# Optimization experiments

Measured on AMD Instinct MI355X. Metric: run time of the kernel, lower is better.

The kernel has to match this reference:

```python
import jax, jax.numpy as jnp
import numpy as np
from jax import lax

B, CIN, H, W = 32, 256, 64, 64
K, STRIDE = 9, 2
CAPS_TYPES, OS0, OS1 = 32, 8, 1
NUM_ITER = 3
OH = (H - K) // STRIDE + 1  # 28
OW = (W - K) // STRIDE + 1  # 28
EPS = 1e-8


def squash(x):
    # Hinton squash over capsule pose dims (os0, os1)
    n2 = jnp.sum(x * x, axis=(-2, -1), keepdims=True)
    return (n2 / (1.0 + n2)) * x / jnp.sqrt(n2 + EPS)


def setup_inputs() -> dict:
    key = jax.random.key(0)
    k1, k2 = jax.random.split(key)
    x = jax.random.normal(k1, (B, CIN, H, W), jnp.float32)
    cout = CAPS_TYPES * OS0 * OS1
    conv_w = jax.random.normal(k2, (cout, CIN, K, K), jnp.float32) / np.float32(np.sqrt(CIN * K * K))
    conv_b = jnp.zeros((cout,), jnp.float32)
    routing_bias = jnp.full((CAPS_TYPES, OH, OW, OS0, OS1), 0.1, jnp.float32)
    return {"x": x, "conv_w": conv_w, "conv_b": conv_b, "routing_bias": routing_bias}


def reference(x, conv_w, conv_b, routing_bias):
    b = x.shape[0]
    caps = lax.conv_general_dilated(
        x, conv_w, (STRIDE, STRIDE), 'VALID',
        dimension_numbers=('NCHW', 'OIHW', 'NCHW'))
    caps = caps + conv_b[None, :, None, None]
    # [b, C*os0*os1, oh, ow] -> [b, C, oh, ow, os0, os1]
    caps = caps.reshape(b, CAPS_TYPES, OS0, OS1, OH, OW).transpose(0, 1, 4, 5, 2, 3)
    poses = squash(caps)
    # Dynamic routing (degenerate: one vote per output capsule, singleton input dims)
    votes = poses  # [b, C, oh, ow, os0, os1]
    logits = jnp.zeros((b, CAPS_TYPES, OH, OW), caps.dtype)
    for _ in range(NUM_ITER):
        c = jax.nn.softmax(logits, axis=1)           # couplings over output caps types
        s = c[..., None, None] * votes + routing_bias  # weighted vote sum (+ bias)
        poses = squash(s)
        logits = logits + jnp.sum(votes * poses, axis=(-2, -1))  # agreement update
    acts = jnp.sqrt(jnp.sum(poses * poses, axis=(-2, -1)))  # [b, C, oh, ow]
    return poses, acts
```

## Files before the change

kernel.cpp:

```cpp
#include <hip/hip_runtime.h>

#define B_    32
#define CIN_  256
#define H_    64
#define W_    64
#define OH_   28
#define OW_   28
#define M_TOTAL 25088
#define POSE_ELEMS 6422528

typedef _Float16 f16;
typedef _Float16 f16x8 __attribute__((ext_vector_type(8)));
typedef _Float16 f16x4 __attribute__((ext_vector_type(4)));
typedef float    f32x4 __attribute__((ext_vector_type(4)));

#define GLD_LDS16(gp, lp) __builtin_amdgcn_global_load_lds( \
    (const __attribute__((address_space(1))) void*)(gp),    \
    (__attribute__((address_space(3))) void*)(lp), 16, 0, 0)

#define SBAR()    asm volatile("s_barrier" ::: "memory")
#define WAITVM2() asm volatile("s_waitcnt vmcnt(2)" ::: "memory")
#define WAITVM4() asm volatile("s_waitcnt vmcnt(4)" ::: "memory")

__global__ __launch_bounds__(256) void xt_kernel(const float* __restrict__ x,
                                                 f16* __restrict__ Xt)
{
    __shared__ float tile[64 * 65];
    const int t  = threadIdx.x;
    const int c0 = blockIdx.x * 64;
    const int h  = blockIdx.y;
    const int b  = blockIdx.z;

    const float* src = x + (((long)(b * CIN_ + c0)) * H_ + h) * W_;
    const int ci = t >> 6, w = t & 63;
#pragma unroll
    for (int it = 0; it < 16; ++it) {
        const int c = it * 4 + ci;
        tile[c * 65 + w] = src[(long)c * (H_ * W_) + w];
    }
    __syncthreads();

    f16* dst = Xt + ((long)(b * H_ + h) * W_) * CIN_ + c0;
    const int wq = t >> 4, cq = t & 15;
#pragma unroll
    for (int it = 0; it < 4; ++it) {
        const int w2 = it * 16 + wq;
        f16x4 v;
        v[0] = (f16)tile[(cq * 4 + 0) * 65 + w2];
        v[1] = (f16)tile[(cq * 4 + 1) * 65 + w2];
        v[2] = (f16)tile[(cq * 4 + 2) * 65 + w2];
        v[3] = (f16)tile[(cq * 4 + 3) * 65 + w2];
        *(f16x4*)(dst + (long)w2 * CIN_ + cq * 4) = v;
    }
}

__global__ __launch_bounds__(256) void wt_kernel(const float* __restrict__ w,
                                                 f16* __restrict__ Wt)
{
    __shared__ float tile[64 * 81];
    const int t  = threadIdx.x;
    const int co = blockIdx.x >> 2;
    const int c0 = (blockIdx.x & 3) * 64;
    const float* src = w + ((long)co * 256 + c0) * 81;
    for (int i = t; i < 64 * 81; i += 256) tile[i] = src[i];
    __syncthreads();
    for (int i = t; i < 64 * 81; i += 256) {
        const int khw = i >> 6, ci = i & 63;
        Wt[(long)khw * 65536 + co * 256 + c0 + ci] = (f16)tile[ci * 81 + khw];
    }
}

__global__ __launch_bounds__(512, 2) void gemm_kernel(const f16* __restrict__ Xt,
                                                      const f16* __restrict__ Wt,
                                                      float* __restrict__ part,
                                                      int nsplit)
{
    __shared__ __align__(16) char lds[131072];
    char* ldsA = lds;
    char* ldsB = lds + 65536;

    const int t    = threadIdx.x;
    const int lane = t & 63, wave = t >> 6;

    const int nwg = 98 * nsplit;
    const int q = nwg >> 3, r8 = nwg & 7;
    const int xcd = blockIdx.x & 7, idx = blockIdx.x >> 3;
    const int wgid = (xcd < r8 ? xcd * (q + 1) : r8 * (q + 1) + (xcd - r8) * q) + idx;
    const int sk = wgid / 98;
    const int mt = wgid - sk * 98;
    const int m0 = mt * 256;

    const int ntb = 324 / nsplit, rem = 324 - ntb * nsplit;
    const int ksb = sk * ntb + (sk < rem ? sk : rem);
    const int NT  = ntb + (sk < rem ? 1 : 0);

    const int csrc = ((lane & 7) ^ (lane >> 3)) * 8;
    int aoff[4], boff[4];
#pragma unroll
    for (int i = 0; i < 4; ++i) {
        const int r  = (i * 8 + wave) * 8 + (lane >> 3);
        const int ga = (r & 63) + ((r >> 6) & 1) * 128 + (r >> 7) * 64;
        const int m  = m0 + ga;
        const int b   = m / 784;
        const int rem2 = m - b * 784;
        const int oh  = rem2 / 28;
        const int ow  = rem2 - oh * 28;
        aoff[i] = ((b * 64 + 2 * oh) * 64 + 2 * ow) * 256 + csrc;
        const int gb = (r & 31) + ((r >> 5) & 3) * 64 + (r >> 7) * 32;
        boff[i] = gb * 256 + csrc;
    }

    const int wm = wave >> 2, wn = wave & 3;
    int rowA[8], rowB[4];
#pragma unroll
    for (int mf = 0; mf < 8; ++mf) {
        const int g  = wm * 128 + mf * 16 + (lane & 15);
        const int lr = (g & 63) + ((g >> 6) & 1) * 128 + (g >> 7) * 64;
        rowA[mf] = lr * 128;
    }
#pragma unroll
    for (int nf = 0; nf < 4; ++nf) {
        const int g  = wn * 64 + nf * 16 + (lane & 15);
        const int lr = (g & 31) + ((g >> 6) << 5) + ((g >> 5) & 1) * 128;
        rowB[nf] = lr * 128;
    }
    int csw[2];
    csw[0] = ((lane >> 4) * 16) ^ ((lane & 7) << 4);
    csw[1] = 64 ^ csw[0];

    f32x4 acc[8][4];
    const f32x4 z = {0.f, 0.f, 0.f, 0.f};
#pragma unroll
    for (int i = 0; i < 8; ++i)
#pragma unroll
        for (int j = 0; j < 4; ++j) acc[i][j] = z;

#define KOFFS(KS, AK, BK)                                      \
    {  const int cb_ = (KS) & 3, khw_ = (KS) >> 2;             \
       const int kh_ = khw_ / 9, kw_ = khw_ - kh_ * 9;         \
       AK = (kh_ * 64 + kw_) * 256 + cb_ * 64;                 \
       BK = khw_ * 65536 + cb_ * 64; }

#define STAGE_A_HALF(H, AK, NB) do {                                               \
    GLD_LDS16(Xt + aoff[2*(H)]   + (AK), ldsA + (NB)*32768 + ((2*(H))*8   + wave)*1024); \
    GLD_LDS16(Xt + aoff[2*(H)+1] + (AK), ldsA + (NB)*32768 + ((2*(H)+1)*8 + wave)*1024); } while(0)
#define STAGE_B_HALF(H, BK, NB) do {                                               \
    GLD_LDS16(Wt + boff[2*(H)]   + (BK), ldsB + (NB)*32768 + ((2*(H))*8   + wave)*1024); \
    GLD_LDS16(Wt + boff[2*(H)+1] + (BK), ldsB + (NB)*32768 + ((2*(H)+1)*8 + wave)*1024); } while(0)

#define MFMA_PAIR(MI, NI, A, Bf)                                                        \
    acc[MI][NI] = __builtin_amdgcn_mfma_f32_16x16x32_f16((A)[0], (Bf)[0], acc[MI][NI], 0,0,0); \
    acc[MI][NI] = __builtin_amdgcn_mfma_f32_16x16x32_f16((A)[1], (Bf)[1], acc[MI][NI], 0,0,0);
#define MFMA_Q(MH, NH, BF)                                          \
    MFMA_PAIR((MH)*4+0, (NH)*2+0, af[0], BF[0]) MFMA_PAIR((MH)*4+0, (NH)*2+1, af[0], BF[1]) \
    MFMA_PAIR((MH)*4+1, (NH)*2+0, af[1], BF[0]) MFMA_PAIR((MH)*4+1, (NH)*2+1, af[1], BF[1]) \
    MFMA_PAIR((MH)*4+2, (NH)*2+0, af[2], BF[0]) MFMA_PAIR((MH)*4+2, (NH)*2+1, af[2], BF[1]) \
    MFMA_PAIR((MH)*4+3, (NH)*2+0, af[3], BF[0]) MFMA_PAIR((MH)*4+3, (NH)*2+1, af[3], BF[1])

#define READ_AF(P, MH) do {                                           \
    _Pragma("unroll")                                                 \
    for (int k_ = 0; k_ < 4; ++k_) {                                  \
        af[k_][0] = *(const f16x8*)((P) + rowA[(MH)*4+k_] + csw[0]);  \
        af[k_][1] = *(const f16x8*)((P) + rowA[(MH)*4+k_] + csw[1]);  \
    } } while(0)
#define READ_BF(P, V, NH) do {                                        \
    _Pragma("unroll")                                                 \
    for (int k_ = 0; k_ < 2; ++k_) {                                  \
        V[k_][0] = *(const f16x8*)((P) + rowB[(NH)*2+k_] + csw[0]);   \
        V[k_][1] = *(const f16x8*)((P) + rowB[(NH)*2+k_] + csw[1]);   \
    } } while(0)

    f16x8 af[4][2], bf0[2][2], bf1[2][2];

    {
        int ak0, bk0;
        KOFFS(ksb, ak0, bk0);
        STAGE_A_HALF(0, ak0, 0);
        STAGE_B_HALF(0, bk0, 0);
        STAGE_A_HALF(1, ak0, 0);
        STAGE_B_HALF(1, bk0, 0);
    }
    WAITVM4();
    SBAR();
    READ_AF(ldsA, 0);
    READ_BF(ldsB, bf0, 0);

#pragma unroll 1
    for (int tt = 0; tt < NT; ++tt) {
        const int c = tt & 1, nc = c ^ 1;
        const int ksn = ksb + ((tt + 1 < NT) ? tt + 1 : tt);
        int akn, bkn;
        KOFFS(ksn, akn, bkn);
        const char* pA  = ldsA + c * 32768;
        const char* pB  = ldsB + c * 32768;
        const char* pAn = ldsA + nc * 32768;
        const char* pBn = ldsB + nc * 32768;

        STAGE_A_HALF(0, akn, nc);
        WAITVM2();
        SBAR();
        READ_BF(pB, bf1, 1);
        __builtin_amdgcn_s_setprio(1);
        MFMA_Q(0, 0, bf0)
        __builtin_amdgcn_s_setprio(0);

        STAGE_B_HALF(0, bkn, nc);
        SBAR();
        __builtin_amdgcn_s_setprio(1);
        MFMA_Q(0, 1, bf1)
        __builtin_amdgcn_s_setprio(0);
        READ_AF(pA, 1);

        STAGE_A_HALF(1, akn, nc);
        SBAR();
        __builtin_amdgcn_s_setprio(1);
        MFMA_Q(1, 1, bf1)
        __builtin_amdgcn_s_setprio(0);

        STAGE_B_HALF(1, bkn, nc);
        WAITVM4();
        SBAR();
        __builtin_amdgcn_s_setprio(1);
        MFMA_Q(1, 0, bf0)
        __builtin_amdgcn_s_setprio(0);
        READ_AF(pAn, 0);
        READ_BF(pBn, bf0, 0);
    }

    float* base = part + (long)sk * (M_TOTAL * 256);
    const int lrow = (lane >> 4) * 4;
#pragma unroll
    for (int nf = 0; nf < 4; ++nf) {
        const int n = wn * 64 + nf * 16 + (lane & 15);
#pragma unroll
        for (int mf = 0; mf < 8; ++mf) {
            const long mrow = m0 + wm * 128 + mf * 16 + lrow;
            float* cw = base + mrow * 256 + n;
#pragma unroll
            for (int j = 0; j < 4; ++j) cw[(long)j * 256] = acc[mf][nf][j];
        }
    }
}

__global__ __launch_bounds__(256) void routing_kernel(const float* __restrict__ part,
                                                      const float* __restrict__ bias,
                                                      const float* __restrict__ rb,
                                                      float* __restrict__ out, int nsplit)
{
    const int t   = threadIdx.x;
    const int m   = blockIdx.x * 8 + (t >> 5);
    const int cap = t & 31;
    const int b   = m / 784;
    const int rem = m - b * 784;
    const int oh  = rem / 28;
    const int ow  = rem - oh * 28;

    const float4 b0 = ((const float4*)(bias + cap * 8))[0];
    const float4 b1 = ((const float4*)(bias + cap * 8))[1];
    float v[8] = {b0.x, b0.y, b0.z, b0.w, b1.x, b1.y, b1.z, b1.w};
#pragma unroll 1
    for (int sk = 0; sk < nsplit; ++sk) {
        const float4* cp = (const float4*)(part + (long)sk * (M_TOTAL * 256) + (long)m * 256 + cap * 8);
        const float4 u0 = cp[0], u1 = cp[1];
        v[0] += u0.x; v[1] += u0.y; v[2] += u0.z; v[3] += u0.w;
        v[4] += u1.x; v[5] += u1.y; v[6] += u1.z; v[7] += u1.w;
    }

    float n2 = 0.f;
#pragma unroll
    for (int j = 0; j < 8; ++j) n2 += v[j] * v[j];
    const float f = (n2 / (1.f + n2)) / sqrtf(n2 + 1e-8f);
    float votes[8];
#pragma unroll
    for (int j = 0; j < 8; ++j) votes[j] = f * v[j];

    const float4* rp = (const float4*)(rb + ((long)(cap * 28 + oh) * 28 + ow) * 8);
    const float4 r0 = rp[0], r1 = rp[1];
    const float rbv[8] = {r0.x, r0.y, r0.z, r0.w, r1.x, r1.y, r1.z, r1.w};

    float logit = 0.f;
    float poses[8];
#pragma unroll 1
    for (int it = 0; it < 3; ++it) {
        float mx = logit;
#pragma unroll
        for (int d = 16; d > 0; d >>= 1) mx = fmaxf(mx, __shfl_xor(mx, d, 32));
        const float e = __expf(logit - mx);
        float se = e;
#pragma unroll
        for (int d = 16; d > 0; d >>= 1) se += __shfl_xor(se, d, 32);
        const float c = e / se;

        float s[8];
        float sn2 = 0.f;
#pragma unroll
        for (int j = 0; j < 8; ++j) { s[j] = c * votes[j] + rbv[j]; sn2 += s[j] * s[j]; }
        const float sf = (sn2 / (1.f + sn2)) / sqrtf(sn2 + 1e-8f);
        float dot = 0.f;
#pragma unroll
        for (int j = 0; j < 8; ++j) { poses[j] = sf * s[j]; dot += votes[j] * poses[j]; }
        logit += dot;
    }

    float pn2 = 0.f;
#pragma unroll
    for (int j = 0; j < 8; ++j) pn2 += poses[j] * poses[j];
    const float act = sqrtf(pn2);

    float* po = out + (((long)(b * 32 + cap) * 28 + oh) * 28 + ow) * 8;
    float4 o0 = {poses[0], poses[1], poses[2], poses[3]};
    float4 o1 = {poses[4], poses[5], poses[6], poses[7]};
    ((float4*)po)[0] = o0;
    ((float4*)po)[1] = o1;
    out[POSE_ELEMS + ((long)(b * 32 + cap) * 28 + oh) * 28 + ow] = act;
}

extern "C" void kernel_launch(void* const* d_in, const int* in_sizes, int n_in,
                              void* d_out, int out_size, void* d_ws, size_t ws_size,
                              hipStream_t stream)
{
    const float* x      = (const float*)d_in[0];
    const float* conv_w = (const float*)d_in[1];
    const float* conv_b = (const float*)d_in[2];
    const float* rb     = (const float*)d_in[3];
    float* out          = (float*)d_out;

    char* ws = (char*)d_ws;
    f16*   Xt   = (f16*)ws;
    f16*   Wt   = (f16*)(ws + 67108864);
    const size_t base = 67108864 + 10616832;
    float* part = (float*)(ws + base);
    const size_t part_bytes = (size_t)M_TOTAL * 256 * 4;

    int nsplit = 1;
    if      (ws_size >= base + 5 * part_bytes) nsplit = 5;
    else if (ws_size >= base + 4 * part_bytes) nsplit = 4;
    else if (ws_size >= base + 2 * part_bytes) nsplit = 2;

    xt_kernel<<<dim3(4, 64, 32), 256, 0, stream>>>(x, Xt);
    wt_kernel<<<dim3(1024), 256, 0, stream>>>(conv_w, Wt);
    gemm_kernel<<<dim3(98 * nsplit), dim3(512), 0, stream>>>(Xt, Wt, part, nsplit);
    routing_kernel<<<dim3(3136), 256, 0, stream>>>(part, conv_b, rb, out, nsplit);
}
```

Measured before the change: 309.4 us.

## Double-buffer A fragments and reorder staging to prefetch next tile earlier

Adds a second register buffer for A fragments so the next tile's first A half can be read from LDS while the current tile's MFMAs still run. The staging order of A and B halves is changed and the vmcnt waits are adjusted to match. A final vmcnt(0) wait is added before the epilogue. The aim is to hide LDS read latency behind MFMA work, at the cost of extra VGPRs and a different barrier and wait schedule that could race or lower occupancy.

```diff
diff --git a/kernel.cpp b/kernel.cpp
--- a/kernel.cpp
+++ b/kernel.cpp
@@ -19,6 +19,7 @@
     (__attribute__((address_space(3))) void*)(lp), 16, 0, 0)
 
 #define SBAR()    asm volatile("s_barrier" ::: "memory")
+#define WAITVM0() asm volatile("s_waitcnt vmcnt(0)" ::: "memory")
 #define WAITVM2() asm volatile("s_waitcnt vmcnt(2)" ::: "memory")
 #define WAITVM4() asm volatile("s_waitcnt vmcnt(4)" ::: "memory")
 
@@ -151,17 +152,17 @@
 #define MFMA_PAIR(MI, NI, A, Bf)                                                        \
     acc[MI][NI] = __builtin_amdgcn_mfma_f32_16x16x32_f16((A)[0], (Bf)[0], acc[MI][NI], 0,0,0); \
     acc[MI][NI] = __builtin_amdgcn_mfma_f32_16x16x32_f16((A)[1], (Bf)[1], acc[MI][NI], 0,0,0);
-#define MFMA_Q(MH, NH, BF)                                          \
-    MFMA_PAIR((MH)*4+0, (NH)*2+0, af[0], BF[0]) MFMA_PAIR((MH)*4+0, (NH)*2+1, af[0], BF[1]) \
-    MFMA_PAIR((MH)*4+1, (NH)*2+0, af[1], BF[0]) MFMA_PAIR((MH)*4+1, (NH)*2+1, af[1], BF[1]) \
-    MFMA_PAIR((MH)*4+2, (NH)*2+0, af[2], BF[0]) MFMA_PAIR((MH)*4+2, (NH)*2+1, af[2], BF[1]) \
-    MFMA_PAIR((MH)*4+3, (NH)*2+0, af[3], BF[0]) MFMA_PAIR((MH)*4+3, (NH)*2+1, af[3], BF[1])
-
-#define READ_AF(P, MH) do {                                           \
+#define MFMA_Q(MH, NH, AF, BF)                                          \
+    MFMA_PAIR((MH)*4+0, (NH)*2+0, AF[0], BF[0]) MFMA_PAIR((MH)*4+0, (NH)*2+1, AF[0], BF[1]) \
+    MFMA_PAIR((MH)*4+1, (NH)*2+0, AF[1], BF[0]) MFMA_PAIR((MH)*4+1, (NH)*2+1, AF[1], BF[1]) \
+    MFMA_PAIR((MH)*4+2, (NH)*2+0, AF[2], BF[0]) MFMA_PAIR((MH)*4+2, (NH)*2+1, AF[2], BF[1]) \
+    MFMA_PAIR((MH)*4+3, (NH)*2+0, AF[3], BF[0]) MFMA_PAIR((MH)*4+3, (NH)*2+1, AF[3], BF[1])
+
+#define READ_AF(P, V, MH) do {                                        \
     _Pragma("unroll")                                                 \
     for (int k_ = 0; k_ < 4; ++k_) {                                  \
-        af[k_][0] = *(const f16x8*)((P) + rowA[(MH)*4+k_] + csw[0]);  \
-        af[k_][1] = *(const f16x8*)((P) + rowA[(MH)*4+k_] + csw[1]);  \
+        V[k_][0] = *(const f16x8*)((P) + rowA[(MH)*4+k_] + csw[0]);   \
+        V[k_][1] = *(const f16x8*)((P) + rowA[(MH)*4+k_] + csw[1]);   \
     } } while(0)
 #define READ_BF(P, V, NH) do {                                        \
     _Pragma("unroll")                                                 \
@@ -170,19 +171,19 @@
         V[k_][1] = *(const f16x8*)((P) + rowB[(NH)*2+k_] + csw[1]);   \
     } } while(0)
 
-    f16x8 af[4][2], bf0[2][2], bf1[2][2];
+    f16x8 af2[4][2], af[4][2], bf0[2][2], bf1[2][2];
 
     {
         int ak0, bk0;
         KOFFS(ksb, ak0, bk0);
         STAGE_A_HALF(0, ak0, 0);
         STAGE_B_HALF(0, bk0, 0);
+        STAGE_B_HALF(1, bk0, 0);
         STAGE_A_HALF(1, ak0, 0);
-        STAGE_B_HALF(1, bk0, 0);
     }
     WAITVM4();
     SBAR();
-    READ_AF(ldsA, 0);
+    READ_AF(ldsA, af2, 0);
     READ_BF(ldsB, bf0, 0);
 
 #pragma unroll 1
@@ -197,35 +198,37 @@
         const char* pBn = ldsB + nc * 32768;
 
         STAGE_A_HALF(0, akn, nc);
-        WAITVM2();
+        WAITVM4();
         SBAR();
         READ_BF(pB, bf1, 1);
         __builtin_amdgcn_s_setprio(1);
-        MFMA_Q(0, 0, bf0)
+        MFMA_Q(0, 0, af2, bf0)
         __builtin_amdgcn_s_setprio(0);
 
         STAGE_B_HALF(0, bkn, nc);
+        WAITVM2();
         SBAR();
+        READ_AF(pA, af, 1);
         __builtin_amdgcn_s_setprio(1);
-        MFMA_Q(0, 1, bf1)
+        MFMA_Q(0, 1, af2, bf1)
         __builtin_amdgcn_s_setprio(0);
-        READ_AF(pA, 1);
+
+        STAGE_B_HALF(1, bkn, nc);
+        SBAR();
+        READ_AF(pAn, af2, 0);
+        __builtin_amdgcn_s_setprio(1);
+        MFMA_Q(1, 1, af, bf1)
+        __builtin_amdgcn_s_setprio(0);
 
         STAGE_A_HALF(1, akn, nc);
-        SBAR();
-        __builtin_amdgcn_s_setprio(1);
-        MFMA_Q(1, 1, bf1)
-        __builtin_amdgcn_s_setprio(0);
-
-        STAGE_B_HALF(1, bkn, nc);
         WAITVM4();
         SBAR();
         __builtin_amdgcn_s_setprio(1);
-        MFMA_Q(1, 0, bf0)
+        MFMA_Q(1, 0, af, bf0)
         __builtin_amdgcn_s_setprio(0);
-        READ_AF(pAn, 0);
         READ_BF(pBn, bf0, 0);
     }
+    WAITVM0();
 
     float* base = part + (long)sk * (M_TOTAL * 256);
     const int lrow = (lane >> 4) * 4;
```

New measurement: 421.3 us. 36.2% more time.
